# Kernel optimization log

Hardware: AMD Instinct MI355X
Metric: run time of the kernel (lower is better)

Reference implementation:

```python
import jax, jax.numpy as jnp
import numpy as np

B, N, L, E = 4, 8, 2048, 16384
CH = [128, 256, 256, 256]
EPS = 1e-5
USE_MAX = True


def setup_inputs() -> dict:
    key = jax.random.key(0)
    ks = jax.random.split(key, 10)
    d = {}
    d["x"] = jax.random.normal(ks[0], (B, N, CH[0], L), jnp.float32)
    d["edge_index"] = jax.random.randint(ks[1], (2, E), 0, L, dtype=jnp.int32)
    wspecs = [("W1", CH[0], CH[1]), ("W2", CH[1], CH[2]), ("W3", CH[2], CH[3]),
              ("W1s", CH[0], CH[1]), ("W2s", CH[1], CH[2]), ("W3s", CH[2], CH[3])]
    for i, (nm, ci, co) in enumerate(wspecs):
        std = (2.0 / (ci + co)) ** 0.5  # xavier_normal
        d[nm] = std * jax.random.normal(ks[2 + i], (ci, co), jnp.float32)
        d["b" + nm[1:]] = jnp.zeros((co,), jnp.float32)
    for nm, co in [("1", CH[1]), ("2", CH[2]), ("3", CH[3]),
                   ("1s", CH[1]), ("2s", CH[2]), ("3s", CH[3])]:
        d["g" + nm] = jnp.ones((co,), jnp.float32)
        d["be" + nm] = jnp.zeros((co,), jnp.float32)
    return d


def _gcn_norm(edge_index, num_nodes):
    # PyG gcn_norm with improved=True: A_hat = A + 2I, sym normalization.
    src, dst = edge_index[0], edge_index[1]
    loop = jnp.arange(num_nodes, dtype=src.dtype)
    src = jnp.concatenate([src, loop])
    dst = jnp.concatenate([dst, loop])
    w = jnp.concatenate([jnp.ones((edge_index.shape[1],), jnp.float32),
                         jnp.full((num_nodes,), 2.0, jnp.float32)])
    deg = jnp.zeros((num_nodes,), jnp.float32).at[dst].add(w)
    dis = jnp.where(deg > 0, jax.lax.rsqrt(deg), 0.0)
    return src, dst, dis[src] * w * dis[dst]


def _gcn(h, W, bias, src, dst, norm, num_nodes):
    # h: [G, L, Cin] node features for G independent copies of the shared graph
    hw = h @ W  # [G, L, Cout]
    msgs = hw[:, src, :] * norm[None, :, None]  # gather along nodes
    agg = jnp.zeros((h.shape[0], num_nodes, W.shape[1]), h.dtype).at[:, dst].add(msgs)
    return agg + bias


def _bn(x, g, be):
    # x: [Nb, C, L]; training-mode BatchNorm1d over (Nb, L) per channel
    m = x.mean(axis=(0, 2), keepdims=True)
    v = x.var(axis=(0, 2), keepdims=True)
    return g[None, :, None] * (x - m) * jax.lax.rsqrt(v + EPS) + be[None, :, None]


def _forward(x, edge_index, params):
    b, n, c, l = x.shape
    src, dst, norm = _gcn_norm(edge_index, l)
    xo = None
    for (W, bias, Ws, bs, g, be, gs, bes) in params:
        # per-element branch
        h = x.reshape(b * n, x.shape[2], l).transpose(0, 2, 1)  # [b*n, L, C]
        x1 = _gcn(h, W, bias, src, dst, norm, l).transpose(0, 2, 1)  # [b*n, Cout, L]
        x1 = _bn(x1, g, be)
        # symmetric pooled branch
        xp = jnp.max(x, axis=1) if USE_MAX else jnp.sum(x, axis=1)  # [b, C, L]
        x2 = _gcn(xp.transpose(0, 2, 1), Ws, bs, src, dst, norm, l).transpose(0, 2, 1)
        x2 = _bn(x2, gs, bes)
        co = x2.shape[1]
        x2 = jnp.broadcast_to(x2[:, None], (b, n, co, l)).reshape(b * n, co, l)
        xo = jax.nn.relu(x1 + x2)  # [b*n, Cout, L]
        x = xo.reshape(b, n, co, l)
    return xo  # final output is [b*n, CH[3], L] (not reshaped back)


def reference(x, edge_index, W1, b1, W2, b2, W3, b3, W1s, b1s, W2s, b2s, W3s, b3s,
              g1, be1, g2, be2, g3, be3, g1s, be1s, g2s, be2s, g3s, be3s):
    params = [(W1, b1, W1s, b1s, g1, be1, g1s, be1s),
              (W2, b2, W2s, b2s, g2, be2, g2s, be2s),
              (W3, b3, W3s, b3s, g3, be3, g3s, be3s)]
    return _forward(x, edge_index, params)
```

## Files before the change

kernel.cpp:

```cpp
#include <hip/hip_runtime.h>
#include <math.h>

#define LNODES 2048
#define NEDGE 16384
#define GBIG 32
#define GSM 4
#define NCOUT 256
#define BN_EPS 1e-5f
#define ND 32

typedef unsigned short u16;
typedef __attribute__((ext_vector_type(8))) short bf16x8;
typedef __attribute__((ext_vector_type(4))) float f32x4;

__device__ __forceinline__ unsigned pk2(float a, float b) {
  unsigned ua = __float_as_uint(a); ua += 0x7fffu + ((ua >> 16) & 1u);
  unsigned ub = __float_as_uint(b); ub += 0x7fffu + ((ub >> 16) & 1u);
  return (ua >> 16) | (ub & 0xffff0000u);
}
__device__ __forceinline__ float blo(unsigned u) { return __uint_as_float(u << 16); }
__device__ __forceinline__ float bhi(unsigned u) { return __uint_as_float(u & 0xffff0000u); }


__global__ __launch_bounds__(256) void count_deg_k(const int* __restrict__ ei,
// ... 84 lines not shown
  const float* src[6];
  u16* dst[6];
  int ci[6];
};
__global__ __launch_bounds__(256) void cvtw_all_k(WCvt wp) {
  __shared__ float T[64][65];
  const int w = blockIdx.z;
  const int Ci = wp.ci[w];
  const int ci0 = blockIdx.y * 64;
  if (ci0 >= Ci) return;
  const float* W = wp.src[w];
  u16* WT = wp.dst[w];
  const int co0 = blockIdx.x * 64;
  const int tr = threadIdx.x >> 4;
  const int tc = (threadIdx.x & 15) * 4;
#pragma unroll
  for (int p = 0; p < 4; ++p) {
    int ci = ci0 + tr + p * 16;
    float4 v = *reinterpret_cast<const float4*>(&W[(size_t)ci * NCOUT + co0 + tc]);
    T[tr + p * 16][tc + 0] = v.x; T[tr + p * 16][tc + 1] = v.y;
    T[tr + p * 16][tc + 2] = v.z; T[tr + p * 16][tc + 3] = v.w;
  }
  __syncthreads();
#pragma unroll
  for (int p = 0; p < 4; ++p) {
    int co = tr + p * 16;
    uint2 o = {pk2(T[tc + 0][co], T[tc + 1][co]), pk2(T[tc + 2][co], T[tc + 3][co])};
    *reinterpret_cast<uint2*>(&WT[(size_t)(co0 + co) * Ci + ci0 + tc]) = o;
  }
}

__global__ __launch_bounds__(256) void pool_bf_k(const u16* __restrict__ X,
                                                 u16* __restrict__ XP, int per) {
  int i = blockIdx.x * 256 + threadIdx.x;
  size_t f = (size_t)i * 8;
  int b = (int)(f / per);
  size_t rem = f - (size_t)b * per;
  const u16* base = X + (size_t)b * 8 * per + rem;
  uint4 u = *reinterpret_cast<const uint4*>(base);
  float m0 = blo(u.x), m1 = bhi(u.x), m2 = blo(u.y), m3 = bhi(u.y);
  float m4 = blo(u.z), m5 = bhi(u.z), m6 = blo(u.w), m7 = bhi(u.w);
#pragma unroll
  for (int j = 1; j < 8; ++j) {
    uint4 v = *reinterpret_cast<const uint4*>(base + (size_t)j * per);
    m0 = fmaxf(m0, blo(v.x)); m1 = fmaxf(m1, bhi(v.x));
    m2 = fmaxf(m2, blo(v.y)); m3 = fmaxf(m3, bhi(v.y));
    m4 = fmaxf(m4, blo(v.z)); m5 = fmaxf(m5, bhi(v.z));
    m6 = fmaxf(m6, blo(v.w)); m7 = fmaxf(m7, bhi(v.w));
  }
  uint4 o = {pk2(m0, m1), pk2(m2, m3), pk2(m4, m5), pk2(m6, m7)};
  *reinterpret_cast<uint4*>(XP + (size_t)b * per + rem) = o;
}

__global__ __launch_bounds__(256) void poolonly_k(const u16* __restrict__ A1,
                                                  const u16* __restrict__ A2,
                                                  const float* __restrict__ k1,
                                                  const float* __restrict__ k2,
                                                  const float* __restrict__ cc,
                                                  u16* __restrict__ XP) {
  const int b = blockIdx.y;
  size_t f = ((size_t)blockIdx.x * 256 + threadIdx.x) * 8;
  int co = (int)(f & (NCOUT - 1));
  float4 K1a = *reinterpret_cast<const float4*>(&k1[co]);
  float4 K1b = *reinterpret_cast<const float4*>(&k1[co + 4]);
  float4 K2a = *reinterpret_cast<const float4*>(&k2[co]);
  float4 K2b = *reinterpret_cast<const float4*>(&k2[co + 4]);
  float4 Ca = *reinterpret_cast<const float4*>(&cc[co]);
  float4 Cb = *reinterpret_cast<const float4*>(&cc[co + 4]);
  uint4 a2 = *reinterpret_cast<const uint4*>(&A2[(size_t)b * LNODES * NCOUT + f]);
  float t0 = K2a.x * blo(a2.x) + Ca.x, t1 = K2a.y * bhi(a2.x) + Ca.y;
  float t2 = K2a.z * blo(a2.y) + Ca.z, t3 = K2a.w * bhi(a2.y) + Ca.w;
  float t4 = K2b.x * blo(a2.z) + Cb.x, t5 = K2b.y * bhi(a2.z) + Cb.y;
  float t6 = K2b.z * blo(a2.w) + Cb.z, t7 = K2b.w * bhi(a2.w) + Cb.w;
  float m0 = 0.f, m1 = 0.f, m2 = 0.f, m3 = 0.f, m4 = 0.f, m5 = 0.f, m6 = 0.f, m7 = 0.f;
#pragma unroll
  for (int n = 0; n < 8; ++n) {
    size_t gi = ((size_t)(b * 8 + n) * LNODES * NCOUT) + f;
    uint4 a1 = *reinterpret_cast<const uint4*>(&A1[gi]);
    m0 = fmaxf(m0, K1a.x * blo(a1.x) + t0);
    m1 = fmaxf(m1, K1a.y * bhi(a1.x) + t1);
    m2 = fmaxf(m2, K1a.z * blo(a1.y) + t2);
    m3 = fmaxf(m3, K1a.w * bhi(a1.y) + t3);
    m4 = fmaxf(m4, K1b.x * blo(a1.z) + t4);
    m5 = fmaxf(m5, K1b.y * bhi(a1.z) + t5);
    m6 = fmaxf(m6, K1b.z * blo(a1.w) + t6);
    m7 = fmaxf(m7, K1b.w * bhi(a1.w) + t7);
  }
  m0 = fmaxf(m0, 0.f); m1 = fmaxf(m1, 0.f); m2 = fmaxf(m2, 0.f); m3 = fmaxf(m3, 0.f);
  m4 = fmaxf(m4, 0.f); m5 = fmaxf(m5, 0.f); m6 = fmaxf(m6, 0.f); m7 = fmaxf(m7, 0.f);
  uint4 mu = {pk2(m0, m1), pk2(m2, m3), pk2(m4, m5), pk2(m6, m7)};
  *reinterpret_cast<uint4*>(&XP[(size_t)b * LNODES * NCOUT + f]) = mu;
}

template <int MODE>
__global__ __launch_bounds__(256) void gemm_all_k(const u16* __restrict__ Xbig,
                                                  const u16* __restrict__ AGG1,
                                                  const u16* __restrict__ agg2,
                                                  const float* __restrict__ k1,
                                                  const float* __restrict__ k2,
                                                  const float* __restrict__ cc,
                                                  const u16* __restrict__ xp,
                                                  const u16* __restrict__ WbT,
                                                  const u16* __restrict__ WsT,
                                                  u16* __restrict__ HW1,
                                                  u16* __restrict__ hw2,
                                                  int CinBig) {
  __shared__ u16 smem[17408];
  __shared__ float lk1[NCOUT], lk2[NCOUT], lcc[NCOUT];
  u16* Wsh = smem;
  u16* Xsh = smem + 128 * 40;
  const int z = blockIdx.z;
  const bool big = z < GBIG;
  const int g = big ? z : z - GBIG;
  const int Cin = big ? CinBig : ((MODE == 0) ? CinBig : NCOUT);
  const u16* Wmat = big ? WbT : WsT;
  u16* out = big ? HW1 : hw2;
  const int n0 = blockIdx.x * 128;
  const int c0 = blockIdx.y * 128;
  const int t = threadIdx.x;
  lk1[t] = k1[t]; lk2[t] = k2[t]; lcc[t] = cc[t];
  __syncthreads();
  const int wv = t >> 6;
  const int lane = t & 63;
  const int q = lane >> 4, l = lane & 15;
  const int wm = wv >> 1, wn = wv & 1;
  f32x4 zero = {0.f, 0.f, 0.f, 0.f};
  f32x4 acc[4][4];
#pragma unroll
  for (int i = 0; i < 4; ++i)
#pragma unroll
    for (int j = 0; j < 4; ++j) acc[i][j] = zero;
  const int r0 = t >> 2;
  const int seg = (t & 3) * 8;
  const u16* Wg = Wmat + (size_t)(c0 + r0) * Cin + seg;
  const u16* Xplain = (big ? Xbig : xp);
  const u16* Xg = Xplain + ((size_t)g * LNODES + n0 + r0) * Cin + seg;
  const size_t a1base = ((size_t)g * LNODES + n0 + r0) * NCOUT + seg;
  const size_t a2base = ((size_t)(g >> 3) * LNODES + n0 + r0) * NCOUT + seg;
  const bool fuse = (MODE == 1) && big;
  for (int k0 = 0; k0 < Cin; k0 += 32) {
    uint4 w0 = *reinterpret_cast<const uint4*>(Wg + k0);
    uint4 w1 = *reinterpret_cast<const uint4*>(Wg + (size_t)64 * Cin + k0);
    uint4 x0, x1;
    if (fuse) {
      uint4 a1a = *reinterpret_cast<const uint4*>(&AGG1[a1base + k0]);
      uint4 a1b = *reinterpret_cast<const uint4*>(&AGG1[a1base + (size_t)64 * NCOUT + k0]);
      uint4 a2a = *reinterpret_cast<const uint4*>(&agg2[a2base + k0]);
      uint4 a2b = *reinterpret_cast<const uint4*>(&agg2[a2base + (size_t)64 * NCOUT + k0]);
      int kk = k0 + seg;
      float o0 = fmaxf(lk1[kk+0]*blo(a1a.x) + lk2[kk+0]*blo(a2a.x) + lcc[kk+0], 0.f);
      float o1 = fmaxf(lk1[kk+1]*bhi(a1a.x) + lk2[kk+1]*bhi(a2a.x) + lcc[kk+1], 0.f);
      float o2 = fmaxf(lk1[kk+2]*blo(a1a.y) + lk2[kk+2]*blo(a2a.y) + lcc[kk+2], 0.f);
      float o3 = fmaxf(lk1[kk+3]*bhi(a1a.y) + lk2[kk+3]*bhi(a2a.y) + lcc[kk+3], 0.f);
      float o4 = fmaxf(lk1[kk+4]*blo(a1a.z) + lk2[kk+4]*blo(a2a.z) + lcc[kk+4], 0.f);
      float o5 = fmaxf(lk1[kk+5]*bhi(a1a.z) + lk2[kk+5]*bhi(a2a.z) + lcc[kk+5], 0.f);
      float o6 = fmaxf(lk1[kk+6]*blo(a1a.w) + lk2[kk+6]*blo(a2a.w) + lcc[kk+6], 0.f);
      float o7 = fmaxf(lk1[kk+7]*bhi(a1a.w) + lk2[kk+7]*bhi(a2a.w) + lcc[kk+7], 0.f);
      x0 = {pk2(o0, o1), pk2(o2, o3), pk2(o4, o5), pk2(o6, o7)};
      float p0 = fmaxf(lk1[kk+0]*blo(a1b.x) + lk2[kk+0]*blo(a2b.x) + lcc[kk+0], 0.f);
      float p1 = fmaxf(lk1[kk+1]*bhi(a1b.x) + lk2[kk+1]*bhi(a2b.x) + lcc[kk+1], 0.f);
      float p2 = fmaxf(lk1[kk+2]*blo(a1b.y) + lk2[kk+2]*blo(a2b.y) + lcc[kk+2], 0.f);
      float p3 = fmaxf(lk1[kk+3]*bhi(a1b.y) + lk2[kk+3]*bhi(a2b.y) + lcc[kk+3], 0.f);
      float p4 = fmaxf(lk1[kk+4]*blo(a1b.z) + lk2[kk+4]*blo(a2b.z) + lcc[kk+4], 0.f);
      float p5 = fmaxf(lk1[kk+5]*bhi(a1b.z) + lk2[kk+5]*bhi(a2b.z) + lcc[kk+5], 0.f);
      float p6 = fmaxf(lk1[kk+6]*blo(a1b.w) + lk2[kk+6]*blo(a2b.w) + lcc[kk+6], 0.f);
      float p7 = fmaxf(lk1[kk+7]*bhi(a1b.w) + lk2[kk+7]*bhi(a2b.w) + lcc[kk+7], 0.f);
      x1 = {pk2(p0, p1), pk2(p2, p3), pk2(p4, p5), pk2(p6, p7)};
    } else {
      x0 = *reinterpret_cast<const uint4*>(Xg + k0);
      x1 = *reinterpret_cast<const uint4*>(Xg + (size_t)64 * Cin + k0);
    }
    __syncthreads();
    *reinterpret_cast<uint4*>(&Wsh[r0 * 40 + seg]) = w0;
    *reinterpret_cast<uint4*>(&Wsh[(r0 + 64) * 40 + seg]) = w1;
    *reinterpret_cast<uint4*>(&Xsh[r0 * 40 + seg]) = x0;
    *reinterpret_cast<uint4*>(&Xsh[(r0 + 64) * 40 + seg]) = x1;
    __syncthreads();
    bf16x8 af[4], bx[4];
#pragma unroll
    for (int fi = 0; fi < 4; ++fi)
      af[fi] = *reinterpret_cast<const bf16x8*>(&Wsh[(wm * 64 + fi * 16 + l) * 40 + q * 8]);
#pragma unroll
    for (int fj = 0; fj < 4; ++fj)
      bx[fj] = *reinterpret_cast<const bf16x8*>(&Xsh[(wn * 64 + fj * 16 + l) * 40 + q * 8]);
#pragma unroll
    for (int fi = 0; fi < 4; ++fi)
#pragma unroll
      for (int fj = 0; fj < 4; ++fj)
        acc[fi][fj] = __builtin_amdgcn_mfma_f32_16x16x32_bf16(af[fi], bx[fj], acc[fi][fj], 0, 0, 0);
  }
  __syncthreads();
  u16* Csh = smem;
#pragma unroll
  for (int fi = 0; fi < 4; ++fi) {
#pragma unroll
    for (int fj = 0; fj < 4; ++fj) {
      int co_l = wm * 64 + fi * 16 + q * 4;
      int nd_l = wn * 64 + fj * 16 + l;
      uint2 pkd = {pk2(acc[fi][fj][0], acc[fi][fj][1]),
                   pk2(acc[fi][fj][2], acc[fi][fj][3])};
      *reinterpret_cast<uint2*>(&Csh[nd_l * 136 + co_l]) = pkd;
    }
  }
  __syncthreads();
#pragma unroll
  for (int p = 0; p < 8; ++p) {
    int idx = p * 256 + t;
    int nd = idx >> 4;
    int c8 = (idx & 15) * 8;
    uint4 v = *reinterpret_cast<const uint4*>(&Csh[nd * 136 + c8]);
    *reinterpret_cast<uint4*>(&out[((size_t)g * LNODES + n0 + nd) * NCOUT + c0 + c8]) = v;
  }
}

__global__ __launch_bounds__(256) void agg_comb_k(const u16* __restrict__ HW1,
                                                  const u16* __restrict__ hw2,
                                                  const int* __restrict__ col,
                                                  const float* __restrict__ wn,
                                                  const int* __restrict__ rp,
                                                  const float* __restrict__ selfn,
                                                  u16* __restrict__ AGG1,
                                                  u16* __restrict__ agg2,
                                                  float* __restrict__ sum1,
                                                  float* __restrict__ sq1,
                                                  float* __restrict__ sum2,
                                                  float* __restrict__ sq2) {
  __shared__ float lsum[4][NCOUT], lsq[4][NCOUT];
  const int bid = blockIdx.x;
  const int t = threadIdx.x;
  const int wv = t >> 6;
  const int lc = (t & 63) * 4;
  float4 s = {0.f, 0.f, 0.f, 0.f}, qq = {0.f, 0.f, 0.f, 0.f};
  float* sumO;
  float* sqO;
  int shard;
  if (bid < 1024) {
    int slot = bid >> 3;
    int chunk = slot & 63;
    int g0 = (bid & 7) + 8 * (slot >> 6);
    const int d0 = chunk * ND;
    const u16* base0 = HW1 + (size_t)g0 * LNODES * NCOUT;
    const u16* base1 = base0 + (size_t)16 * LNODES * NCOUT;
    for (int i = wv; i < ND; i += 4) {
      int d = d0 + i;
      int e0 = rp[d], e1 = rp[d + 1];
      float sw = selfn[d];
      uint2 u0 = *reinterpret_cast<const uint2*>(&base0[(size_t)d * NCOUT + lc]);
      uint2 u1 = *reinterpret_cast<const uint2*>(&base1[(size_t)d * NCOUT + lc]);
      float4 a = {sw * blo(u0.x), sw * bhi(u0.x), sw * blo(u0.y), sw * bhi(u0.y)};
      float4 c = {sw * blo(u1.x), sw * bhi(u1.x), sw * blo(u1.y), sw * bhi(u1.y)};
      int e = e0;
      const int e4 = e0 + ((e1 - e0) & ~3);
      for (; e < e4; e += 4) {
        int i0 = col[e + 0], i1 = col[e + 1], i2 = col[e + 2], i3 = col[e + 3];
        float w0 = wn[e + 0], w1 = wn[e + 1], w2 = wn[e + 2], w3 = wn[e + 3];
        uint2 v0 = *reinterpret_cast<const uint2*>(&base0[(size_t)i0 * NCOUT + lc]);
        uint2 v1 = *reinterpret_cast<const uint2*>(&base0[(size_t)i1 * NCOUT + lc]);
        uint2 v2 = *reinterpret_cast<const uint2*>(&base0[(size_t)i2 * NCOUT + lc]);
        uint2 v3 = *reinterpret_cast<const uint2*>(&base0[(size_t)i3 * NCOUT + lc]);
        uint2 p0 = *reinterpret_cast<const uint2*>(&base1[(size_t)i0 * NCOUT + lc]);
        uint2 p1 = *reinterpret_cast<const uint2*>(&base1[(size_t)i1 * NCOUT + lc]);
        uint2 p2 = *reinterpret_cast<const uint2*>(&base1[(size_t)i2 * NCOUT + lc]);
        uint2 p3 = *reinterpret_cast<const uint2*>(&base1[(size_t)i3 * NCOUT + lc]);
        a.x += w0 * blo(v0.x); a.y += w0 * bhi(v0.x); a.z += w0 * blo(v0.y); a.w += w0 * bhi(v0.y);
        a.x += w1 * blo(v1.x); a.y += w1 * bhi(v1.x); a.z += w1 * blo(v1.y); a.w += w1 * bhi(v1.y);
        a.x += w2 * blo(v2.x); a.y += w2 * bhi(v2.x); a.z += w2 * blo(v2.y); a.w += w2 * bhi(v2.y);
        a.x += w3 * blo(v3.x); a.y += w3 * bhi(v3.x); a.z += w3 * blo(v3.y); a.w += w3 * bhi(v3.y);
        c.x += w0 * blo(p0.x); c.y += w0 * bhi(p0.x); c.z += w0 * blo(p0.y); c.w += w0 * bhi(p0.y);
        c.x += w1 * blo(p1.x); c.y += w1 * bhi(p1.x); c.z += w1 * blo(p1.y); c.w += w1 * bhi(p1.y);
        c.x += w2 * blo(p2.x); c.y += w2 * bhi(p2.x); c.z += w2 * blo(p2.y); c.w += w2 * bhi(p2.y);
        c.x += w3 * blo(p3.x); c.y += w3 * bhi(p3.x); c.z += w3 * blo(p3.y); c.w += w3 * bhi(p3.y);
      }
      for (; e < e1; ++e) {
        int ci = col[e];
        float w = wn[e];
        uint2 v = *reinterpret_cast<const uint2*>(&base0[(size_t)ci * NCOUT + lc]);
        uint2 pv = *reinterpret_cast<const uint2*>(&base1[(size_t)ci * NCOUT + lc]);
        a.x += w * blo(v.x); a.y += w * bhi(v.x); a.z += w * blo(v.y); a.w += w * bhi(v.y);
        c.x += w * blo(pv.x); c.y += w * bhi(pv.x); c.z += w * blo(pv.y); c.w += w * bhi(pv.y);
      }
      uint2 o0 = {pk2(a.x, a.y), pk2(a.z, a.w)};
      *reinterpret_cast<uint2*>(&AGG1[((size_t)g0 * LNODES + d) * NCOUT + lc]) = o0;
      uint2 o1 = {pk2(c.x, c.y), pk2(c.z, c.w)};
      *reinterpret_cast<uint2*>(&AGG1[((size_t)(g0 + 16) * LNODES + d) * NCOUT + lc]) = o1;
      s.x += a.x + c.x; s.y += a.y + c.y; s.z += a.z + c.z; s.w += a.w + c.w;
      qq.x += a.x * a.x + c.x * c.x; qq.y += a.y * a.y + c.y * c.y;
      qq.z += a.z * a.z + c.z * c.z; qq.w += a.w * a.w + c.w * c.w;
    }
    sumO = sum1; sqO = sq1; shard = (bid & 7) * NCOUT;
  } else {
    int b2 = bid - 1024;
    int g = b2 & (GSM - 1);
    int chunk = b2 >> 2;
    const int d0 = chunk * ND;
    const u16* base = hw2 + (size_t)g * LNODES * NCOUT;
    for (int i = wv; i < ND; i += 4) {
      int d = d0 + i;
      int e0 = rp[d], e1 = rp[d + 1];
      float sw = selfn[d];
      uint2 u = *reinterpret_cast<const uint2*>(&base[(size_t)d * NCOUT + lc]);
      float4 a = {sw * blo(u.x), sw * bhi(u.x), sw * blo(u.y), sw * bhi(u.y)};
      int e = e0;
      const int e4 = e0 + ((e1 - e0) & ~3);
      for (; e < e4; e += 4) {
        int i0 = col[e + 0], i1 = col[e + 1], i2 = col[e + 2], i3 = col[e + 3];
        float w0 = wn[e + 0], w1 = wn[e + 1], w2 = wn[e + 2], w3 = wn[e + 3];
        uint2 v0 = *reinterpret_cast<const uint2*>(&base[(size_t)i0 * NCOUT + lc]);
        uint2 v1 = *reinterpret_cast<const uint2*>(&base[(size_t)i1 * NCOUT + lc]);
        uint2 v2 = *reinterpret_cast<const uint2*>(&base[(size_t)i2 * NCOUT + lc]);
        uint2 v3 = *reinterpret_cast<const uint2*>(&base[(size_t)i3 * NCOUT + lc]);
        a.x += w0 * blo(v0.x); a.y += w0 * bhi(v0.x); a.z += w0 * blo(v0.y); a.w += w0 * bhi(v0.y);
        a.x += w1 * blo(v1.x); a.y += w1 * bhi(v1.x); a.z += w1 * blo(v1.y); a.w += w1 * bhi(v1.y);
        a.x += w2 * blo(v2.x); a.y += w2 * bhi(v2.x); a.z += w2 * blo(v2.y); a.w += w2 * bhi(v2.y);
        a.x += w3 * blo(v3.x); a.y += w3 * bhi(v3.x); a.z += w3 * blo(v3.y); a.w += w3 * bhi(v3.y);
      }
      for (; e < e1; ++e) {
        float w = wn[e];
        uint2 v = *reinterpret_cast<const uint2*>(&base[(size_t)col[e] * NCOUT + lc]);
        a.x += w * blo(v.x); a.y += w * bhi(v.x); a.z += w * blo(v.y); a.w += w * bhi(v.y);
      }
      uint2 o = {pk2(a.x, a.y), pk2(a.z, a.w)};
      *reinterpret_cast<uint2*>(&agg2[((size_t)g * LNODES + d) * NCOUT + lc]) = o;
      s.x += a.x; s.y += a.y; s.z += a.z; s.w += a.w;
      qq.x += a.x * a.x; qq.y += a.y * a.y; qq.z += a.z * a.z; qq.w += a.w * a.w;
    }
    sumO = sum2; sqO = sq2; shard = (b2 & 7) * NCOUT;
  }
  *reinterpret_cast<float4*>(&lsum[wv][lc]) = s;
  *reinterpret_cast<float4*>(&lsq[wv][lc]) = qq;
  __syncthreads();
  float ts = lsum[0][t] + lsum[1][t] + lsum[2][t] + lsum[3][t];
  float tq = lsq[0][t] + lsq[1][t] + lsq[2][t] + lsq[3][t];
  atomicAdd(&sumO[shard + t], ts);
  atomicAdd(&sqO[shard + t], tq);
}

__global__ __launch_bounds__(256) void bnfinal_k(float* __restrict__ sum1,
                                                 float* __restrict__ sq1,
                                                 float* __restrict__ sum2,
                                                 float* __restrict__ sq2,
                                                 const float* __restrict__ ga,
                                                 const float* __restrict__ be,
                                                 const float* __restrict__ gs,
                                                 const float* __restrict__ bes,
                                                 float* __restrict__ k1,
                                                 float* __restrict__ k2,
                                                 float* __restrict__ cc) {
  int co = threadIdx.x;
  float sA = 0.f, qA = 0.f, sB = 0.f, qB = 0.f;
#pragma unroll
  for (int x = 0; x < 8; ++x) {
    sA += sum1[x * NCOUT + co];
    qA += sq1[x * NCOUT + co];
    sB += sum2[x * NCOUT + co];
    qB += sq2[x * NCOUT + co];
    sum1[x * NCOUT + co] = 0.f;
    sq1[x * NCOUT + co] = 0.f;
    sum2[x * NCOUT + co] = 0.f;
    sq2[x * NCOUT + co] = 0.f;
  }
  const float c1 = (float)(GBIG * LNODES), c2 = (float)(GSM * LNODES);
  float mA = sA / c1;
  float vA = qA / c1 - mA * mA;
  float kA = ga[co] * rsqrtf(vA + BN_EPS);
  float mB = sB / c2;
  float vB = qB / c2 - mB * mB;
  float kB = gs[co] * rsqrtf(vB + BN_EPS);
  k1[co] = kA;
  k2[co] = kB;
  cc[co] = be[co] - kA * mA + bes[co] - kB * mB;
}

__global__ __launch_bounds__(256) void fuse_tr_bf_k(const u16* __restrict__ A1,
                                                    const u16* __restrict__ A2,
                                                    const float* __restrict__ k1,
                                                    const float* __restrict__ k2,
                                                    const float* __restrict__ cc,
                                                    float* __restrict__ O) {
  __shared__ float T[64][65];
  const int g = blockIdx.z;
  const int d0 = blockIdx.x * 64;
  const int c0 = blockIdx.y * 64;
  const int b = g >> 3;
  const int tr = threadIdx.x >> 4;
  const int tc = (threadIdx.x & 15) * 4;
  float4 K1 = *reinterpret_cast<const float4*>(&k1[c0 + tc]);
  float4 K2 = *reinterpret_cast<const float4*>(&k2[c0 + tc]);
  float4 CC = *reinterpret_cast<const float4*>(&cc[c0 + tc]);
#pragma unroll
  for (int p = 0; p < 4; ++p) {
    int d = d0 + tr + p * 16;
    uint2 a1 = *reinterpret_cast<const uint2*>(&A1[((size_t)g * LNODES + d) * NCOUT + c0 + tc]);
    uint2 a2 = *reinterpret_cast<const uint2*>(&A2[((size_t)b * LNODES + d) * NCOUT + c0 + tc]);
    T[tr + p * 16][tc + 0] = fmaxf(K1.x * blo(a1.x) + K2.x * blo(a2.x) + CC.x, 0.f);
    T[tr + p * 16][tc + 1] = fmaxf(K1.y * bhi(a1.x) + K2.y * bhi(a2.x) + CC.y, 0.f);
    T[tr + p * 16][tc + 2] = fmaxf(K1.z * blo(a1.y) + K2.z * blo(a2.y) + CC.z, 0.f);
    T[tr + p * 16][tc + 3] = fmaxf(K1.w * bhi(a1.y) + K2.w * bhi(a2.y) + CC.w, 0.f);
  }
  __syncthreads();
#pragma unroll
  for (int p = 0; p < 4; ++p) {
    int c = tr + p * 16;
    float4 o = {T[tc + 0][c], T[tc + 1][c], T[tc + 2][c], T[tc + 3][c]};
    *reinterpret_cast<float4*>(&O[((size_t)g * NCOUT + c0 + c) * LNODES + d0 + tc]) = o;
  }
}


extern "C" void kernel_launch(void* const* d_in, const int* in_sizes, int n_in,
                              void* d_out, int out_size, void* d_ws, size_t ws_size,
                              hipStream_t stream) {
  const float* x_in = (const float*)d_in[0];
  const int* ei = (const int*)d_in[1];
  const float* W[3]   = {(const float*)d_in[2],  (const float*)d_in[4],  (const float*)d_in[6]};
  const float* Wsym[3]= {(const float*)d_in[8],  (const float*)d_in[10], (const float*)d_in[12]};
  const float* ga[3]  = {(const float*)d_in[14], (const float*)d_in[16], (const float*)d_in[18]};
  const float* be[3]  = {(const float*)d_in[15], (const float*)d_in[17], (const float*)d_in[19]};
  const float* gs[3]  = {(const float*)d_in[20], (const float*)d_in[22], (const float*)d_in[24]};
  const float* bes[3] = {(const float*)d_in[21], (const float*)d_in[23], (const float*)d_in[25]};

  const size_t EBIG = (size_t)GBIG * LNODES * NCOUT;
  const size_t ESM = (size_t)GSM * LNODES * NCOUT;
  char* p = (char*)d_ws;
  u16* XT0  = (u16*)p; p += (size_t)GBIG * LNODES * 128 * 2;
  u16* AGG1 = (u16*)p; p += EBIG * 2;
  u16* agg2 = (u16*)p; p += ESM * 2;
  u16* xp   = (u16*)p; p += ESM * 2;
  u16* hw2  = (u16*)p; p += ESM * 2;
  u16* WbT[3], *WsT[3];
  for (int i = 0; i < 3; ++i) { WbT[i] = (u16*)p; p += NCOUT * NCOUT * 2; }
  for (int i = 0; i < 3; ++i) { WsT[i] = (u16*)p; p += NCOUT * NCOUT * 2; }
  int*   col  = (int*)p;   p += NEDGE * 4;
  float* wn   = (float*)p; p += NEDGE * 4;
  int*   rp   = (int*)p;   p += 2064 * 4;
  float* dis  = (float*)p; p += LNODES * 4;
  float* selfn= (float*)p; p += LNODES * 4;
  char* zbase = p;
  float* deg  = (float*)p; p += LNODES * 4;
  int*   cnt  = (int*)p;   p += LNODES * 4;
  int*   fillc= (int*)p;   p += LNODES * 4;
  float* sum1 = (float*)p; p += 8 * 1024;
  float* sq1  = (float*)p; p += 8 * 1024;
  float* sum2 = (float*)p; p += 8 * 1024;
  float* sq2  = (float*)p; p += 8 * 1024;
  size_t zsize = (size_t)(p - zbase);
  float* k1 = (float*)p; p += 1024;
  float* k2 = (float*)p; p += 1024;
  float* cc = (float*)p; p += 1024;
  u16* HW1 = (u16*)d_out;

  hipMemsetAsync(zbase, 0, zsize, stream);
  count_deg_k<<<NEDGE / 256, 256, 0, stream>>>(ei, deg, cnt);
  dis_k<<<LNODES / 256, 256, 0, stream>>>(deg, dis, selfn);
  scan_k<<<1, 256, 0, stream>>>(cnt, rp);
  fill_k<<<NEDGE / 256, 256, 0, stream>>>(ei, rp, fillc, dis, col, wn);
  WCvt wc;
  for (int i = 0; i < 3; ++i) {
    wc.src[i] = W[i];     wc.dst[i] = WbT[i];     wc.ci[i] = (i == 0) ? 128 : 256;
    wc.src[3 + i] = Wsym[i]; wc.dst[3 + i] = WsT[i]; wc.ci[3 + i] = (i == 0) ? 128 : 256;
  }
  cvtw_all_k<<<dim3(4, 4, 6), 256, 0, stream>>>(wc);
  trans_k<<<dim3(LNODES / 64, 128 / 64, GBIG), 256, 0, stream>>>(x_in, XT0, 128);
  pool_bf_k<<<GSM * 128 * LNODES / 8 / 256, 256, 0, stream>>>(XT0, xp, 128 * LNODES);

  for (int l = 0; l < 3; ++l) {
    if (l > 0) {
      poolonly_k<<<dim3(256, GSM), 256, 0, stream>>>(AGG1, agg2, k1, k2, cc, xp);
      gemm_all_k<1><<<dim3(LNODES / 128, NCOUT / 128, GBIG + GSM), 256, 0, stream>>>(
          XT0, AGG1, agg2, k1, k2, cc, xp, WbT[l], WsT[l], HW1, hw2, NCOUT);
    } else {
      gemm_all_k<0><<<dim3(LNODES / 128, NCOUT / 128, GBIG + GSM), 256, 0, stream>>>(
          XT0, AGG1, agg2, k1, k2, cc, xp, WbT[l], WsT[l], HW1, hw2, 128);
    }
    agg_comb_k<<<1280, 256, 0, stream>>>(HW1, hw2, col, wn, rp, selfn,
                                         AGG1, agg2, sum1, sq1, sum2, sq2);
    bnfinal_k<<<1, 256, 0, stream>>>(sum1, sq1, sum2, sq2,
                                     ga[l], be[l], gs[l], bes[l], k1, k2, cc);
  }
  fuse_tr_bf_k<<<dim3(LNODES / 64, NCOUT / 64, GBIG), 256, 0, stream>>>(
      AGG1, agg2, k1, k2, cc, (float*)d_out);
}
```

Before: 376.3 us.

## Fuse BN finalize and symmetric pooling into GEMM prologue, drop extra launches

Removes the separate bnfinal and poolonly kernels. Each GEMM block now recomputes the BN scale and shift coefficients from per-layer stats buffers, and the symmetric-branch blocks compute the max-pool over the 8 elements on the fly while loading their input tile. Per-layer stats buffers replace the zero-reset done inside bnfinal, and the edge loop tail becomes a masked 4-wide loop over padded col/wn arrays. This saves launches and one round trip of the pooled tensor through memory, at the cost of redundant coefficient computation per block and heavier sym-block prologues that read 8x more AGG1 data.

```diff
diff --git a/kernel.cpp b/kernel.cpp
--- a/kernel.cpp
+++ b/kernel.cpp
@@ -160,74 +160,63 @@
   *reinterpret_cast<uint4*>(XP + (size_t)b * per + rem) = o;
 }
 
-__global__ __launch_bounds__(256) void poolonly_k(const u16* __restrict__ A1,
-                                                  const u16* __restrict__ A2,
-                                                  const float* __restrict__ k1,
-                                                  const float* __restrict__ k2,
-                                                  const float* __restrict__ cc,
-                                                  u16* __restrict__ XP) {
-  const int b = blockIdx.y;
-  size_t f = ((size_t)blockIdx.x * 256 + threadIdx.x) * 8;
-  int co = (int)(f & (NCOUT - 1));
-  float4 K1a = *reinterpret_cast<const float4*>(&k1[co]);
-  float4 K1b = *reinterpret_cast<const float4*>(&k1[co + 4]);
-  float4 K2a = *reinterpret_cast<const float4*>(&k2[co]);
-  float4 K2b = *reinterpret_cast<const float4*>(&k2[co + 4]);
-  float4 Ca = *reinterpret_cast<const float4*>(&cc[co]);
-  float4 Cb = *reinterpret_cast<const float4*>(&cc[co + 4]);
-  uint4 a2 = *reinterpret_cast<const uint4*>(&A2[(size_t)b * LNODES * NCOUT + f]);
-  float t0 = K2a.x * blo(a2.x) + Ca.x, t1 = K2a.y * bhi(a2.x) + Ca.y;
-  float t2 = K2a.z * blo(a2.y) + Ca.z, t3 = K2a.w * bhi(a2.y) + Ca.w;
-  float t4 = K2b.x * blo(a2.z) + Cb.x, t5 = K2b.y * bhi(a2.z) + Cb.y;
-  float t6 = K2b.z * blo(a2.w) + Cb.z, t7 = K2b.w * bhi(a2.w) + Cb.w;
-  float m0 = 0.f, m1 = 0.f, m2 = 0.f, m3 = 0.f, m4 = 0.f, m5 = 0.f, m6 = 0.f, m7 = 0.f;
-#pragma unroll
-  for (int n = 0; n < 8; ++n) {
-    size_t gi = ((size_t)(b * 8 + n) * LNODES * NCOUT) + f;
-    uint4 a1 = *reinterpret_cast<const uint4*>(&A1[gi]);
-    m0 = fmaxf(m0, K1a.x * blo(a1.x) + t0);
-    m1 = fmaxf(m1, K1a.y * bhi(a1.x) + t1);
-    m2 = fmaxf(m2, K1a.z * blo(a1.y) + t2);
-    m3 = fmaxf(m3, K1a.w * bhi(a1.y) + t3);
-    m4 = fmaxf(m4, K1b.x * blo(a1.z) + t4);
-    m5 = fmaxf(m5, K1b.y * bhi(a1.z) + t5);
-    m6 = fmaxf(m6, K1b.z * blo(a1.w) + t6);
-    m7 = fmaxf(m7, K1b.w * bhi(a1.w) + t7);
-  }
-  m0 = fmaxf(m0, 0.f); m1 = fmaxf(m1, 0.f); m2 = fmaxf(m2, 0.f); m3 = fmaxf(m3, 0.f);
-  m4 = fmaxf(m4, 0.f); m5 = fmaxf(m5, 0.f); m6 = fmaxf(m6, 0.f); m7 = fmaxf(m7, 0.f);
-  uint4 mu = {pk2(m0, m1), pk2(m2, m3), pk2(m4, m5), pk2(m6, m7)};
-  *reinterpret_cast<uint4*>(&XP[(size_t)b * LNODES * NCOUT + f]) = mu;
+__device__ __forceinline__ void coef_ld(const float* __restrict__ st,
+                                        const float* __restrict__ ga,
+                                        const float* __restrict__ be,
+                                        const float* __restrict__ gs,
+                                        const float* __restrict__ bes,
+                                        float* lk1, float* lk2, float* lcc, int t) {
+  float sA = 0.f, qA = 0.f, sB = 0.f, qB = 0.f;
+#pragma unroll
+  for (int x = 0; x < 8; ++x) {
+    sA += st[x * NCOUT + t];
+    qA += st[2048 + x * NCOUT + t];
+    sB += st[4096 + x * NCOUT + t];
+    qB += st[6144 + x * NCOUT + t];
+  }
+  const float c1 = (float)(GBIG * LNODES), c2 = (float)(GSM * LNODES);
+  float mA = sA / c1;
+  float vA = qA / c1 - mA * mA;
+  float kA = ga[t] * rsqrtf(vA + BN_EPS);
+  float mB = sB / c2;
+  float vB = qB / c2 - mB * mB;
+  float kB = gs[t] * rsqrtf(vB + BN_EPS);
+  lk1[t] = kA;
+  lk2[t] = kB;
+  lcc[t] = be[t] - kA * mA + bes[t] - kB * mB;
 }
 
 template <int MODE>
 __global__ __launch_bounds__(256) void gemm_all_k(const u16* __restrict__ Xbig,
+                                                  const u16* __restrict__ xp,
                                                   const u16* __restrict__ AGG1,
                                                   const u16* __restrict__ agg2,
-                                                  const float* __restrict__ k1,
-                                                  const float* __restrict__ k2,
-                                                  const float* __restrict__ cc,
-                                                  const u16* __restrict__ xp,
+                                                  const float* __restrict__ st,
+                                                  const float* __restrict__ ga,
+                                                  const float* __restrict__ be,
+                                                  const float* __restrict__ gs,
+                                                  const float* __restrict__ bes,
                                                   const u16* __restrict__ WbT,
                                                   const u16* __restrict__ WsT,
                                                   u16* __restrict__ HW1,
                                                   u16* __restrict__ hw2,
-                                                  int CinBig) {
+                                                  int Cin) {
   __shared__ u16 smem[17408];
   __shared__ float lk1[NCOUT], lk2[NCOUT], lcc[NCOUT];
   u16* Wsh = smem;
   u16* Xsh = smem + 128 * 40;
   const int z = blockIdx.z;
-  const bool big = z < GBIG;
-  const int g = big ? z : z - GBIG;
-  const int Cin = big ? CinBig : ((MODE == 0) ? CinBig : NCOUT);
-  const u16* Wmat = big ? WbT : WsT;
-  u16* out = big ? HW1 : hw2;
+  const bool sym = z < GSM;
+  const int g = sym ? z : z - GSM;
+  const u16* Wmat = sym ? WsT : WbT;
+  u16* out = sym ? hw2 : HW1;
   const int n0 = blockIdx.x * 128;
   const int c0 = blockIdx.y * 128;
   const int t = threadIdx.x;
-  lk1[t] = k1[t]; lk2[t] = k2[t]; lcc[t] = cc[t];
-  __syncthreads();
+  if (MODE == 1) {
+    coef_ld(st, ga, be, gs, bes, lk1, lk2, lcc, t);
+    __syncthreads();
+  }
   const int wv = t >> 6;
   const int lane = t & 63;
   const int q = lane >> 4, l = lane & 15;
@@ -241,42 +230,77 @@
   const int r0 = t >> 2;
   const int seg = (t & 3) * 8;
   const u16* Wg = Wmat + (size_t)(c0 + r0) * Cin + seg;
-  const u16* Xplain = (big ? Xbig : xp);
+  const u16* Xplain = sym ? xp : Xbig;
   const u16* Xg = Xplain + ((size_t)g * LNODES + n0 + r0) * Cin + seg;
-  const size_t a1base = ((size_t)g * LNODES + n0 + r0) * NCOUT + seg;
-  const size_t a2base = ((size_t)(g >> 3) * LNODES + n0 + r0) * NCOUT + seg;
-  const bool fuse = (MODE == 1) && big;
+  const size_t rowd = (size_t)(n0 + r0);
+  const size_t nstep = (size_t)LNODES * NCOUT;
+  const size_t a1base = sym ? (((size_t)(g * 8) * LNODES + rowd) * NCOUT + seg)
+                            : (((size_t)g * LNODES + rowd) * NCOUT + seg);
+  const size_t a2base = sym ? (((size_t)g * LNODES + rowd) * NCOUT + seg)
+                            : (((size_t)(g >> 3) * LNODES + rowd) * NCOUT + seg);
   for (int k0 = 0; k0 < Cin; k0 += 32) {
     uint4 w0 = *reinterpret_cast<const uint4*>(Wg + k0);
     uint4 w1 = *reinterpret_cast<const uint4*>(Wg + (size_t)64 * Cin + k0);
     uint4 x0, x1;
-    if (fuse) {
-      uint4 a1a = *reinterpret_cast<const uint4*>(&AGG1[a1base + k0]);
-      uint4 a1b = *reinterpret_cast<const uint4*>(&AGG1[a1base + (size_t)64 * NCOUT + k0]);
-      uint4 a2a = *reinterpret_cast<const uint4*>(&agg2[a2base + k0]);
-      uint4 a2b = *reinterpret_cast<const uint4*>(&agg2[a2base + (size_t)64 * NCOUT + k0]);
-      int kk = k0 + seg;
-      float o0 = fmaxf(lk1[kk+0]*blo(a1a.x) + lk2[kk+0]*blo(a2a.x) + lcc[kk+0], 0.f);
-      float o1 = fmaxf(lk1[kk+1]*bhi(a1a.x) + lk2[kk+1]*bhi(a2a.x) + lcc[kk+1], 0.f);
-      float o2 = fmaxf(lk1[kk+2]*blo(a1a.y) + lk2[kk+2]*blo(a2a.y) + lcc[kk+2], 0.f);
-      float o3 = fmaxf(lk1[kk+3]*bhi(a1a.y) + lk2[kk+3]*bhi(a2a.y) + lcc[kk+3], 0.f);
-      float o4 = fmaxf(lk1[kk+4]*blo(a1a.z) + lk2[kk+4]*blo(a2a.z) + lcc[kk+4], 0.f);
-      float o5 = fmaxf(lk1[kk+5]*bhi(a1a.z) + lk2[kk+5]*bhi(a2a.z) + lcc[kk+5], 0.f);
-      float o6 = fmaxf(lk1[kk+6]*blo(a1a.w) + lk2[kk+6]*blo(a2a.w) + lcc[kk+6], 0.f);
-      float o7 = fmaxf(lk1[kk+7]*bhi(a1a.w) + lk2[kk+7]*bhi(a2a.w) + lcc[kk+7], 0.f);
-      x0 = {pk2(o0, o1), pk2(o2, o3), pk2(o4, o5), pk2(o6, o7)};
-      float p0 = fmaxf(lk1[kk+0]*blo(a1b.x) + lk2[kk+0]*blo(a2b.x) + lcc[kk+0], 0.f);
-      float p1 = fmaxf(lk1[kk+1]*bhi(a1b.x) + lk2[kk+1]*bhi(a2b.x) + lcc[kk+1], 0.f);
-      float p2 = fmaxf(lk1[kk+2]*blo(a1b.y) + lk2[kk+2]*blo(a2b.y) + lcc[kk+2], 0.f);
-      float p3 = fmaxf(lk1[kk+3]*bhi(a1b.y) + lk2[kk+3]*bhi(a2b.y) + lcc[kk+3], 0.f);
-      float p4 = fmaxf(lk1[kk+4]*blo(a1b.z) + lk2[kk+4]*blo(a2b.z) + lcc[kk+4], 0.f);
-      float p5 = fmaxf(lk1[kk+5]*bhi(a1b.z) + lk2[kk+5]*bhi(a2b.z) + lcc[kk+5], 0.f);
-      float p6 = fmaxf(lk1[kk+6]*blo(a1b.w) + lk2[kk+6]*blo(a2b.w) + lcc[kk+6], 0.f);
-      float p7 = fmaxf(lk1[kk+7]*bhi(a1b.w) + lk2[kk+7]*bhi(a2b.w) + lcc[kk+7], 0.f);
-      x1 = {pk2(p0, p1), pk2(p2, p3), pk2(p4, p5), pk2(p6, p7)};
-    } else {
+    if (MODE == 0) {
       x0 = *reinterpret_cast<const uint4*>(Xg + k0);
       x1 = *reinterpret_cast<const uint4*>(Xg + (size_t)64 * Cin + k0);
+    } else {
+      int kk = k0 + seg;
+      float K10 = lk1[kk+0], K11 = lk1[kk+1], K12 = lk1[kk+2], K13 = lk1[kk+3];
+      float K14 = lk1[kk+4], K15 = lk1[kk+5], K16 = lk1[kk+6], K17 = lk1[kk+7];
+      if (!sym) {
+        uint4 a1a = *reinterpret_cast<const uint4*>(&AGG1[a1base + k0]);
+        uint4 a1b = *reinterpret_cast<const uint4*>(&AGG1[a1base + 64 * (size_t)NCOUT + k0]);
+        uint4 a2a = *reinterpret_cast<const uint4*>(&agg2[a2base + k0]);
+        uint4 a2b = *reinterpret_cast<const uint4*>(&agg2[a2base + 64 * (size_t)NCOUT + k0]);
+        float o0 = fmaxf(K10*blo(a1a.x) + lk2[kk+0]*blo(a2a.x) + lcc[kk+0], 0.f);
+        float o1 = fmaxf(K11*bhi(a1a.x) + lk2[kk+1]*bhi(a2a.x) + lcc[kk+1], 0.f);
+        float o2 = fmaxf(K12*blo(a1a.y) + lk2[kk+2]*blo(a2a.y) + lcc[kk+2], 0.f);
+        float o3 = fmaxf(K13*bhi(a1a.y) + lk2[kk+3]*bhi(a2a.y) + lcc[kk+3], 0.f);
+        float o4 = fmaxf(K14*blo(a1a.z) + lk2[kk+4]*blo(a2a.z) + lcc[kk+4], 0.f);
+        float o5 = fmaxf(K15*bhi(a1a.z) + lk2[kk+5]*bhi(a2a.z) + lcc[kk+5], 0.f);
+        float o6 = fmaxf(K16*blo(a1a.w) + lk2[kk+6]*blo(a2a.w) + lcc[kk+6], 0.f);
+        float o7 = fmaxf(K17*bhi(a1a.w) + lk2[kk+7]*bhi(a2a.w) + lcc[kk+7], 0.f);
+        x0 = {pk2(o0, o1), pk2(o2, o3), pk2(o4, o5), pk2(o6, o7)};
+        float p0 = fmaxf(K10*blo(a1b.x) + lk2[kk+0]*blo(a2b.x) + lcc[kk+0], 0.f);
+        float p1 = fmaxf(K11*bhi(a1b.x) + lk2[kk+1]*bhi(a2b.x) + lcc[kk+1], 0.f);
+        float p2 = fmaxf(K12*blo(a1b.y) + lk2[kk+2]*blo(a2b.y) + lcc[kk+2], 0.f);
+        float p3 = fmaxf(K13*bhi(a1b.y) + lk2[kk+3]*bhi(a2b.y) + lcc[kk+3], 0.f);
+        float p4 = fmaxf(K14*blo(a1b.z) + lk2[kk+4]*blo(a2b.z) + lcc[kk+4], 0.f);
+        float p5 = fmaxf(K15*bhi(a1b.z) + lk2[kk+5]*bhi(a2b.z) + lcc[kk+5], 0.f);
+        float p6 = fmaxf(K16*blo(a1b.w) + lk2[kk+6]*blo(a2b.w) + lcc[kk+6], 0.f);
+        float p7 = fmaxf(K17*bhi(a1b.w) + lk2[kk+7]*bhi(a2b.w) + lcc[kk+7], 0.f);
+        x1 = {pk2(p0, p1), pk2(p2, p3), pk2(p4, p5), pk2(p6, p7)};
+      } else {
+        uint4 a2a = *reinterpret_cast<const uint4*>(&agg2[a2base + k0]);
+        uint4 a2b = *reinterpret_cast<const uint4*>(&agg2[a2base + 64 * (size_t)NCOUT + k0]);
+        float t0 = lk2[kk+0]*blo(a2a.x) + lcc[kk+0], t1 = lk2[kk+1]*bhi(a2a.x) + lcc[kk+1];
+        float t2 = lk2[kk+2]*blo(a2a.y) + lcc[kk+2], t3 = lk2[kk+3]*bhi(a2a.y) + lcc[kk+3];
+        float t4 = lk2[kk+4]*blo(a2a.z) + lcc[kk+4], t5 = lk2[kk+5]*bhi(a2a.z) + lcc[kk+5];
+        float t6 = lk2[kk+6]*blo(a2a.w) + lcc[kk+6], t7 = lk2[kk+7]*bhi(a2a.w) + lcc[kk+7];
+        float u0 = lk2[kk+0]*blo(a2b.x) + lcc[kk+0], u1 = lk2[kk+1]*bhi(a2b.x) + lcc[kk+1];
+        float u2 = lk2[kk+2]*blo(a2b.y) + lcc[kk+2], u3 = lk2[kk+3]*bhi(a2b.y) + lcc[kk+3];
+        float u4 = lk2[kk+4]*blo(a2b.z) + lcc[kk+4], u5 = lk2[kk+5]*bhi(a2b.z) + lcc[kk+5];
+        float u6 = lk2[kk+6]*blo(a2b.w) + lcc[kk+6], u7 = lk2[kk+7]*bhi(a2b.w) + lcc[kk+7];
+        float m0 = 0.f, m1 = 0.f, m2 = 0.f, m3 = 0.f, m4 = 0.f, m5 = 0.f, m6 = 0.f, m7 = 0.f;
+        float e0 = 0.f, e1 = 0.f, e2 = 0.f, e3 = 0.f, e4 = 0.f, e5 = 0.f, e6 = 0.f, e7 = 0.f;
+#pragma unroll
+        for (int n = 0; n < 8; ++n) {
+          uint4 a1a = *reinterpret_cast<const uint4*>(&AGG1[a1base + n * nstep + k0]);
+          uint4 a1b = *reinterpret_cast<const uint4*>(&AGG1[a1base + n * nstep + 64 * (size_t)NCOUT + k0]);
+          m0 = fmaxf(m0, K10*blo(a1a.x) + t0); m1 = fmaxf(m1, K11*bhi(a1a.x) + t1);
+          m2 = fmaxf(m2, K12*blo(a1a.y) + t2); m3 = fmaxf(m3, K13*bhi(a1a.y) + t3);
+          m4 = fmaxf(m4, K14*blo(a1a.z) + t4); m5 = fmaxf(m5, K15*bhi(a1a.z) + t5);
+          m6 = fmaxf(m6, K16*blo(a1a.w) + t6); m7 = fmaxf(m7, K17*bhi(a1a.w) + t7);
+          e0 = fmaxf(e0, K10*blo(a1b.x) + u0); e1 = fmaxf(e1, K11*bhi(a1b.x) + u1);
+          e2 = fmaxf(e2, K12*blo(a1b.y) + u2); e3 = fmaxf(e3, K13*bhi(a1b.y) + u3);
+          e4 = fmaxf(e4, K14*blo(a1b.z) + u4); e5 = fmaxf(e5, K15*bhi(a1b.z) + u5);
+          e6 = fmaxf(e6, K16*blo(a1b.w) + u6); e7 = fmaxf(e7, K17*bhi(a1b.w) + u7);
+        }
+        x0 = {pk2(m0, m1), pk2(m2, m3), pk2(m4, m5), pk2(m6, m7)};
+        x1 = {pk2(e0, e1), pk2(e2, e3), pk2(e4, e5), pk2(e6, e7)};
+      }
     }
     __syncthreads();
     *reinterpret_cast<uint4*>(&Wsh[r0 * 40 + seg]) = w0;
@@ -329,10 +353,7 @@
                                                   const float* __restrict__ selfn,
                                                   u16* __restrict__ AGG1,
                                                   u16* __restrict__ agg2,
-                                                  float* __restrict__ sum1,
-                                                  float* __restrict__ sq1,
-                                                  float* __restrict__ sum2,
-                                                  float* __restrict__ sq2) {
+                                                  float* __restrict__ st) {
   __shared__ float lsum[4][NCOUT], lsq[4][NCOUT];
   const int bid = blockIdx.x;
   const int t = threadIdx.x;
@@ -357,11 +378,12 @@
       uint2 u1 = *reinterpret_cast<const uint2*>(&base1[(size_t)d * NCOUT + lc]);
       float4 a = {sw * blo(u0.x), sw * bhi(u0.x), sw * blo(u0.y), sw * bhi(u0.y)};
       float4 c = {sw * blo(u1.x), sw * bhi(u1.x), sw * blo(u1.y), sw * bhi(u1.y)};
-      int e = e0;
-      const int e4 = e0 + ((e1 - e0) & ~3);
-      for (; e < e4; e += 4) {
+      for (int e = e0; e < e1; e += 4) {
         int i0 = col[e + 0], i1 = col[e + 1], i2 = col[e + 2], i3 = col[e + 3];
-        float w0 = wn[e + 0], w1 = wn[e + 1], w2 = wn[e + 2], w3 = wn[e + 3];
+        float w0 = wn[e + 0];
+        float w1 = (e + 1 < e1) ? wn[e + 1] : 0.f;
+        float w2 = (e + 2 < e1) ? wn[e + 2] : 0.f;
+        float w3 = (e + 3 < e1) ? wn[e + 3] : 0.f;
         uint2 v0 = *reinterpret_cast<const uint2*>(&base0[(size_t)i0 * NCOUT + lc]);
         uint2 v1 = *reinterpret_cast<const uint2*>(&base0[(size_t)i1 * NCOUT + lc]);
         uint2 v2 = *reinterpret_cast<const uint2*>(&base0[(size_t)i2 * NCOUT + lc]);
@@ -379,14 +401,6 @@
         c.x += w2 * blo(p2.x); c.y += w2 * bhi(p2.x); c.z += w2 * blo(p2.y); c.w += w2 * bhi(p2.y);
         c.x += w3 * blo(p3.x); c.y += w3 * bhi(p3.x); c.z += w3 * blo(p3.y); c.w += w3 * bhi(p3.y);
       }
-      for (; e < e1; ++e) {
-        int ci = col[e];
-        float w = wn[e];
-        uint2 v = *reinterpret_cast<const uint2*>(&base0[(size_t)ci * NCOUT + lc]);
-        uint2 pv = *reinterpret_cast<const uint2*>(&base1[(size_t)ci * NCOUT + lc]);
-        a.x += w * blo(v.x); a.y += w * bhi(v.x); a.z += w * blo(v.y); a.w += w * bhi(v.y);
-        c.x += w * blo(pv.x); c.y += w * bhi(pv.x); c.z += w * blo(pv.y); c.w += w * bhi(pv.y);
-      }
       uint2 o0 = {pk2(a.x, a.y), pk2(a.z, a.w)};
       *reinterpret_cast<uint2*>(&AGG1[((size_t)g0 * LNODES + d) * NCOUT + lc]) = o0;
       uint2 o1 = {pk2(c.x, c.y), pk2(c.z, c.w)};
@@ -395,7 +409,7 @@
       qq.x += a.x * a.x + c.x * c.x; qq.y += a.y * a.y + c.y * c.y;
       qq.z += a.z * a.z + c.z * c.z; qq.w += a.w * a.w + c.w * c.w;
     }
-    sumO = sum1; sqO = sq1; shard = (bid & 7) * NCOUT;
+    sumO = st; sqO = st + 2048; shard = (bid & 7) * NCOUT;
   } else {
     int b2 = bid - 1024;
     int g = b2 & (GSM - 1);
@@ -408,11 +422,12 @@
       float sw = selfn[d];
       uint2 u = *reinterpret_cast<const uint2*>(&base[(size_t)d * NCOUT + lc]);
       float4 a = {sw * blo(u.x), sw * bhi(u.x), sw * blo(u.y), sw * bhi(u.y)};
-      int e = e0;
-      const int e4 = e0 + ((e1 - e0) & ~3);
-      for (; e < e4; e += 4) {
+      for (int e = e0; e < e1; e += 4) {
         int i0 = col[e + 0], i1 = col[e + 1], i2 = col[e + 2], i3 = col[e + 3];
-        float w0 = wn[e + 0], w1 = wn[e + 1], w2 = wn[e + 2], w3 = wn[e + 3];
+        float w0 = wn[e + 0];
+        float w1 = (e + 1 < e1) ? wn[e + 1] : 0.f;
+        float w2 = (e + 2 < e1) ? wn[e + 2] : 0.f;
+        float w3 = (e + 3 < e1) ? wn[e + 3] : 0.f;
         uint2 v0 = *reinterpret_cast<const uint2*>(&base[(size_t)i0 * NCOUT + lc]);
         uint2 v1 = *reinterpret_cast<const uint2*>(&base[(size_t)i1 * NCOUT + lc]);
         uint2 v2 = *reinterpret_cast<const uint2*>(&base[(size_t)i2 * NCOUT + lc]);
@@ -422,17 +437,12 @@
         a.x += w2 * blo(v2.x); a.y += w2 * bhi(v2.x); a.z += w2 * blo(v2.y); a.w += w2 * bhi(v2.y);
         a.x += w3 * blo(v3.x); a.y += w3 * bhi(v3.x); a.z += w3 * blo(v3.y); a.w += w3 * bhi(v3.y);
       }
-      for (; e < e1; ++e) {
-        float w = wn[e];
-        uint2 v = *reinterpret_cast<const uint2*>(&base[(size_t)col[e] * NCOUT + lc]);
-        a.x += w * blo(v.x); a.y += w * bhi(v.x); a.z += w * blo(v.y); a.w += w * bhi(v.y);
-      }
       uint2 o = {pk2(a.x, a.y), pk2(a.z, a.w)};
       *reinterpret_cast<uint2*>(&agg2[((size_t)g * LNODES + d) * NCOUT + lc]) = o;
       s.x += a.x; s.y += a.y; s.z += a.z; s.w += a.w;
       qq.x += a.x * a.x; qq.y += a.y * a.y; qq.z += a.z * a.z; qq.w += a.w * a.w;
     }
-    sumO = sum2; sqO = sq2; shard = (b2 & 7) * NCOUT;
+    sumO = st + 4096; sqO = st + 6144; shard = (b2 & 7) * NCOUT;
   }
   *reinterpret_cast<float4*>(&lsum[wv][lc]) = s;
   *reinterpret_cast<float4*>(&lsq[wv][lc]) = qq;
@@ -443,67 +453,35 @@
   atomicAdd(&sqO[shard + t], tq);
 }
 
-__global__ __launch_bounds__(256) void bnfinal_k(float* __restrict__ sum1,
-                                                 float* __restrict__ sq1,
-                                                 float* __restrict__ sum2,
-                                                 float* __restrict__ sq2,
-                                                 const float* __restrict__ ga,
-                                                 const float* __restrict__ be,
-                                                 const float* __restrict__ gs,
-                                                 const float* __restrict__ bes,
-                                                 float* __restrict__ k1,
-                                                 float* __restrict__ k2,
-                                                 float* __restrict__ cc) {
-  int co = threadIdx.x;
-  float sA = 0.f, qA = 0.f, sB = 0.f, qB = 0.f;
-#pragma unroll
-  for (int x = 0; x < 8; ++x) {
-    sA += sum1[x * NCOUT + co];
-    qA += sq1[x * NCOUT + co];
-    sB += sum2[x * NCOUT + co];
-    qB += sq2[x * NCOUT + co];
-    sum1[x * NCOUT + co] = 0.f;
-    sq1[x * NCOUT + co] = 0.f;
-    sum2[x * NCOUT + co] = 0.f;
-    sq2[x * NCOUT + co] = 0.f;
-  }
-  const float c1 = (float)(GBIG * LNODES), c2 = (float)(GSM * LNODES);
-  float mA = sA / c1;
-  float vA = qA / c1 - mA * mA;
-  float kA = ga[co] * rsqrtf(vA + BN_EPS);
-  float mB = sB / c2;
-  float vB = qB / c2 - mB * mB;
-  float kB = gs[co] * rsqrtf(vB + BN_EPS);
-  k1[co] = kA;
-  k2[co] = kB;
-  cc[co] = be[co] - kA * mA + bes[co] - kB * mB;
-}
-
 __global__ __launch_bounds__(256) void fuse_tr_bf_k(const u16* __restrict__ A1,
                                                     const u16* __restrict__ A2,
-                                                    const float* __restrict__ k1,
-                                                    const float* __restrict__ k2,
-                                                    const float* __restrict__ cc,
+                                                    const float* __restrict__ st,
+                                                    const float* __restrict__ ga,
+                                                    const float* __restrict__ be,
+                                                    const float* __restrict__ gs,
+                                                    const float* __restrict__ bes,
                                                     float* __restrict__ O) {
   __shared__ float T[64][65];
+  __shared__ float lk1[NCOUT], lk2[NCOUT], lcc[NCOUT];
   const int g = blockIdx.z;
   const int d0 = blockIdx.x * 64;
   const int c0 = blockIdx.y * 64;
   const int b = g >> 3;
-  const int tr = threadIdx.x >> 4;
-  const int tc = (threadIdx.x & 15) * 4;
-  float4 K1 = *reinterpret_cast<const float4*>(&k1[c0 + tc]);
-  float4 K2 = *reinterpret_cast<const float4*>(&k2[c0 + tc]);
-  float4 CC = *reinterpret_cast<const float4*>(&cc[c0 + tc]);
+  const int t = threadIdx.x;
+  coef_ld(st, ga, be, gs, bes, lk1, lk2, lcc, t);
+  __syncthreads();
+  const int tr = t >> 4;
+  const int tc = (t & 15) * 4;
 #pragma unroll
   for (int p = 0; p < 4; ++p) {
     int d = d0 + tr + p * 16;
     uint2 a1 = *reinterpret_cast<const uint2*>(&A1[((size_t)g * LNODES + d) * NCOUT + c0 + tc]);
     uint2 a2 = *reinterpret_cast<const uint2*>(&A2[((size_t)b * LNODES + d) * NCOUT + c0 + tc]);
-    T[tr + p * 16][tc + 0] = fmaxf(K1.x * blo(a1.x) + K2.x * blo(a2.x) + CC.x, 0.f);
-    T[tr + p * 16][tc + 1] = fmaxf(K1.y * bhi(a1.x) + K2.y * bhi(a2.x) + CC.y, 0.f);
-    T[tr + p * 16][tc + 2] = fmaxf(K1.z * blo(a1.y) + K2.z * blo(a2.y) + CC.z, 0.f);
-    T[tr + p * 16][tc + 3] = fmaxf(K1.w * bhi(a1.y) + K2.w * bhi(a2.y) + CC.w, 0.f);
+    int cb = c0 + tc;
+    T[tr + p * 16][tc + 0] = fmaxf(lk1[cb+0] * blo(a1.x) + lk2[cb+0] * blo(a2.x) + lcc[cb+0], 0.f);
+    T[tr + p * 16][tc + 1] = fmaxf(lk1[cb+1] * bhi(a1.x) + lk2[cb+1] * bhi(a2.x) + lcc[cb+1], 0.f);
+    T[tr + p * 16][tc + 2] = fmaxf(lk1[cb+2] * blo(a1.y) + lk2[cb+2] * blo(a2.y) + lcc[cb+2], 0.f);
+    T[tr + p * 16][tc + 3] = fmaxf(lk1[cb+3] * bhi(a1.y) + lk2[cb+3] * bhi(a2.y) + lcc[cb+3], 0.f);
   }
   __syncthreads();
 #pragma unroll
@@ -533,13 +511,11 @@
   u16* XT0  = (u16*)p; p += (size_t)GBIG * LNODES * 128 * 2;
   u16* AGG1 = (u16*)p; p += EBIG * 2;
   u16* agg2 = (u16*)p; p += ESM * 2;
-  u16* xp   = (u16*)p; p += ESM * 2;
+  u16* xp   = (u16*)p; p += (size_t)GSM * LNODES * 128 * 2;
   u16* hw2  = (u16*)p; p += ESM * 2;
   u16* WbT[3], *WsT[3];
   for (int i = 0; i < 3; ++i) { WbT[i] = (u16*)p; p += NCOUT * NCOUT * 2; }
   for (int i = 0; i < 3; ++i) { WsT[i] = (u16*)p; p += NCOUT * NCOUT * 2; }
-  int*   col  = (int*)p;   p += NEDGE * 4;
-  float* wn   = (float*)p; p += NEDGE * 4;
   int*   rp   = (int*)p;   p += 2064 * 4;
   float* dis  = (float*)p; p += LNODES * 4;
   float* selfn= (float*)p; p += LNODES * 4;
@@ -547,15 +523,13 @@
   float* deg  = (float*)p; p += LNODES * 4;
   int*   cnt  = (int*)p;   p += LNODES * 4;
   int*   fillc= (int*)p;   p += LNODES * 4;
-  float* sum1 = (float*)p; p += 8 * 1024;
-  float* sq1  = (float*)p; p += 8 * 1024;
-  float* sum2 = (float*)p; p += 8 * 1024;
-  float* sq2  = (float*)p; p += 8 * 1024;
+  int*   col  = (int*)p;   p += (NEDGE + 8) * 4;
+  float* wn   = (float*)p; p += (NEDGE + 8) * 4;
+  float* stats= (float*)p; p += 3 * 4 * 2048 * 4;
   size_t zsize = (size_t)(p - zbase);
-  float* k1 = (float*)p; p += 1024;
-  float* k2 = (float*)p; p += 1024;
-  float* cc = (float*)p; p += 1024;
+
   u16* HW1 = (u16*)d_out;
+  float* stL[3] = {stats, stats + 8192, stats + 16384};
 
   hipMemsetAsync(zbase, 0, zsize, stream);
   count_deg_k<<<NEDGE / 256, 256, 0, stream>>>(ei, deg, cnt);
@@ -571,20 +545,20 @@
   trans_k<<<dim3(LNODES / 64, 128 / 64, GBIG), 256, 0, stream>>>(x_in, XT0, 128);
   pool_bf_k<<<GSM * 128 * LNODES / 8 / 256, 256, 0, stream>>>(XT0, xp, 128 * LNODES);
 
+  dim3 ggrid(LNODES / 128, NCOUT / 128, GBIG + GSM);
   for (int l = 0; l < 3; ++l) {
-    if (l > 0) {
-      poolonly_k<<<dim3(256, GSM), 256, 0, stream>>>(AGG1, agg2, k1, k2, cc, xp);
-      gemm_all_k<1><<<dim3(LNODES / 128, NCOUT / 128, GBIG + GSM), 256, 0, stream>>>(
-          XT0, AGG1, agg2, k1, k2, cc, xp, WbT[l], WsT[l], HW1, hw2, NCOUT);
+    if (l == 0) {
+      gemm_all_k<0><<<ggrid, 256, 0, stream>>>(XT0, xp, AGG1, agg2, nullptr,
+                                               nullptr, nullptr, nullptr, nullptr,
+                                               WbT[l], WsT[l], HW1, hw2, 128);
     } else {
-      gemm_all_k<0><<<dim3(LNODES / 128, NCOUT / 128, GBIG + GSM), 256, 0, stream>>>(
-          XT0, AGG1, agg2, k1, k2, cc, xp, WbT[l], WsT[l], HW1, hw2, 128);
+      gemm_all_k<1><<<ggrid, 256, 0, stream>>>(XT0, xp, AGG1, agg2, stL[l - 1],
+                                               ga[l - 1], be[l - 1], gs[l - 1], bes[l - 1],
+                                               WbT[l], WsT[l], HW1, hw2, NCOUT);
     }
     agg_comb_k<<<1280, 256, 0, stream>>>(HW1, hw2, col, wn, rp, selfn,
-                                         AGG1, agg2, sum1, sq1, sum2, sq2);
-    bnfinal_k<<<1, 256, 0, stream>>>(sum1, sq1, sum2, sq2,
-                                     ga[l], be[l], gs[l], bes[l], k1, k2, cc);
+                                         AGG1, agg2, stL[l]);
   }
   fuse_tr_bf_k<<<dim3(LNODES / 64, NCOUT / 64, GBIG), 256, 0, stream>>>(
-      AGG1, agg2, k1, k2, cc, (float*)d_out);
-}
+      AGG1, agg2, stL[2], ga[2], be[2], gs[2], bes[2], (float*)d_out);
+}
```

Result: faster. 367.3 us (-2.4%).
